# Optimization experiments

Hardware: AMD Instinct MI355X
Metric: run time of the kernel (lower is better)

Reference implementation:

```python
import jax, jax.numpy as jnp
import numpy as np

PI = float(np.pi)

def setup_inputs() -> dict:
    key = jax.random.key(0)
    k1, k2 = jax.random.split(key)
    inp = jax.random.normal(k1, (16, 4096, 512), dtype=jnp.float32)
    lengths = jax.random.randint(k2, (16,), 0, 4096, dtype=jnp.int32)
    return {"inp": inp, "lengths": lengths}

def reference(inp, lengths):
    B, S, D = inp.shape
    pos = jnp.arange(S, dtype=jnp.float32)                      # [S]
    lens = lengths.astype(jnp.float32)[:, None]                  # [B,1]
    safe_len = jnp.maximum(lens, 1.0)
    # cos(x / len * pi) for x < len, else 0 (matches torch.zeros init)
    pe = jnp.where(pos[None, :] < lens,
                   jnp.cos(pos[None, :] / safe_len * PI),
                   0.0)                                          # [B,S]
    pe = pe.astype(inp.dtype)
    # original intent: concatenate positional channel along feature dim
    return jnp.concatenate([inp, pe[:, :, None]], axis=2)        # [B,S,D+1]
```

## Files before the change

### kernel.cpp

```cpp
#include <hip/hip_runtime.h>
#include <hip/hip_bf16.h>
#include <math.h>


#define PB 16
#define PS 4096
#define PD 512
#define PI_F 3.14159265358979323846f

__global__ __launch_bounds__(256) void sinpe_kernel(
    const float* __restrict__ inp,
    const int* __restrict__ lengths,
    float* __restrict__ out)
{
    const int row = blockIdx.x;
    const int s   = row & (PS - 1);
    const int b   = row >> 12;

    const float* __restrict__ in_row  = inp + (size_t)row * PD;
    float* __restrict__       out_row = out + (size_t)row * (PD + 1);

    const int t = threadIdx.x;

    out_row[t]       = in_row[t];
    out_row[t + 256] = in_row[t + 256];

    if (t == 0) {
        const int len = lengths[b];
        float pe = 0.0f;
        if (s < len) {
            const float fl = fmaxf((float)len, 1.0f);
            pe = cosf(((float)s / fl) * PI_F);
        }
        out_row[PD] = pe;
    }
}

extern "C" void kernel_launch(void* const* d_in, const int* in_sizes, int n_in,
                              void* d_out, int out_size, void* d_ws, size_t ws_size,
                              hipStream_t stream)
{
    const float* inp     = (const float*)d_in[0];
    const int*   lengths = (const int*)d_in[1];
    float*       out     = (float*)d_out;

    const int n_rows = PB * PS;
    sinpe_kernel<<<n_rows, 256, 0, stream>>>(inp, lengths, out);
}
```

Measured before the change: 222.4 us.

## Process four rows per block with aligned float4 output stores

Each block now handles four rows, whose 2052 output floats form a 16-byte-aligned span. That span is written as 513 float4 stores, and each store gathers its four input values with scalar loads, handling row boundaries and the positional channel in a slow path. The aim is to replace unaligned scalar stores with wide aligned writes and to cut the block count by four. In exchange, input loads stay scalar and misaligned relative to the output, and one thread does a tail iteration on its own.

Result: slower. 233.7 us (+5.0%).

```diff
diff --git a/kernel.cpp b/kernel.cpp
--- a/kernel.cpp
+++ b/kernel.cpp
@@ -1,11 +1,11 @@
 #include <hip/hip_runtime.h>
-#include <hip/hip_bf16.h>
 #include <math.h>
 
 
 #define PB 16
 #define PS 4096
 #define PD 512
+#define PDO 513
 #define PI_F 3.14159265358979323846f
 
 __global__ __launch_bounds__(256) void sinpe_kernel(
@@ -13,27 +13,52 @@
     const int* __restrict__ lengths,
     float* __restrict__ out)
 {
-    const int row = blockIdx.x;
-    const int s   = row & (PS - 1);
-    const int b   = row >> 12;
-
-    const float* __restrict__ in_row  = inp + (size_t)row * PD;
-    float* __restrict__       out_row = out + (size_t)row * (PD + 1);
+    const int blk  = blockIdx.x;
+    const int row0 = blk << 2;
+    const float* __restrict__ in_base = inp + (size_t)row0 * PD;
+    float4* __restrict__ out_base = (float4*)(out + (size_t)row0 * PDO);
 
     const int t = threadIdx.x;
 
-    out_row[t]       = in_row[t];
-    out_row[t + 256] = in_row[t + 256];
+    auto process = [&](int q) {
+        const int l0 = q << 2;
+        const int r  = (l0 >= 3 * PDO) ? 3 : (l0 >= 2 * PDO) ? 2 : (l0 >= PDO) ? 1 : 0;
+        const int c0 = l0 - r * PDO;
 
-    if (t == 0) {
-        const int len = lengths[b];
-        float pe = 0.0f;
-        if (s < len) {
-            const float fl = fmaxf((float)len, 1.0f);
-            pe = cosf(((float)s / fl) * PI_F);
+        float4 v;
+        if (c0 <= PD - 4) {
+            const float* __restrict__ p = in_base + r * PD + c0;
+            v.x = p[0]; v.y = p[1]; v.z = p[2]; v.w = p[3];
+        } else {
+            float tmp[4];
+#pragma unroll
+            for (int j = 0; j < 4; ++j) {
+                int c  = c0 + j;
+                int rr = r;
+                if (c >= PDO) { c -= PDO; ++rr; }
+                if (c < PD) {
+                    tmp[j] = in_base[rr * PD + c];
+                } else {
+                    const int grow = row0 + rr;
+                    const int s    = grow & (PS - 1);
+                    const int b    = grow >> 12;
+                    const int len  = lengths[b];
+                    float pe = 0.0f;
+                    if (s < len) {
+                        const float fl = fmaxf((float)len, 1.0f);
+                        pe = cosf(((float)s / fl) * PI_F);
+                    }
+                    tmp[j] = pe;
+                }
+            }
+            v.x = tmp[0]; v.y = tmp[1]; v.z = tmp[2]; v.w = tmp[3];
         }
-        out_row[PD] = pe;
-    }
+        out_base[q] = v;
+    };
+
+    process(t);
+    process(t + 256);
+    if (t == 0) process(512);
 }
 
 extern "C" void kernel_launch(void* const* d_in, const int* in_sizes, int n_in,
@@ -44,6 +69,6 @@
     const int*   lengths = (const int*)d_in[1];
     float*       out     = (float*)d_out;
 
-    const int n_rows = PB * PS;
-    sinpe_kernel<<<n_rows, 256, 0, stream>>>(inp, lengths, out);
+    const int n_blocks = (PB * PS) / 4;
+    sinpe_kernel<<<n_blocks, 256, 0, stream>>>(inp, lengths, out);
 }
```

## Stage 16 rows in swizzled LDS to emit fully vectorized float4 output

Applied to the files above, without the earlier changes.

Each block now handles 16 rows. It loads the input with float4 reads into registers, writes them into shared memory with an XOR swizzle that avoids bank conflicts, and appends the cosine positional values. It then reassembles the 513-wide output rows so every store is an aligned float4. This removes the misaligned scalar stores that the odd row stride forced and cuts the number of blocks by 16x. The cost is 33KB of LDS per block, a block barrier, and index arithmetic with a magic-number division in the emit loop.

Result: slower. 232.8 us (+4.7%).

```diff
diff --git a/kernel.cpp b/kernel.cpp
--- a/kernel.cpp
+++ b/kernel.cpp
@@ -1,39 +1,96 @@
 #include <hip/hip_runtime.h>
-#include <hip/hip_bf16.h>
 #include <math.h>
 
 
-#define PB 16
-#define PS 4096
-#define PD 512
+#define PB   16
+#define PS   4096
+#define PD   512
+#define PDO  513
+#define ROWS 16
+#define TPB  256
+#define IN_DW  (ROWS * PD)
+#define IMG_DW (IN_DW + ROWS)
+#define OUT_V4 ((ROWS * PDO) / 4)
 #define PI_F 3.14159265358979323846f
 
-__global__ __launch_bounds__(256) void sinpe_kernel(
+__device__ __forceinline__ int phi(int idx) {
+    return idx ^ ((idx >> 5) & 3);
+}
+
+__global__ __launch_bounds__(TPB) void sinpe_kernel(
     const float* __restrict__ inp,
     const int* __restrict__ lengths,
     float* __restrict__ out)
 {
-    const int row = blockIdx.x;
-    const int s   = row & (PS - 1);
-    const int b   = row >> 12;
+    __shared__ float lds[IMG_DW];
 
-    const float* __restrict__ in_row  = inp + (size_t)row * PD;
-    float* __restrict__       out_row = out + (size_t)row * (PD + 1);
+    const int blk  = blockIdx.x;
+    const int row0 = blk * ROWS;
+    const int t    = threadIdx.x;
 
-    const int t = threadIdx.x;
+    const float4* __restrict__ in4  = (const float4*)(inp + (size_t)row0 * PD);
+    float4* __restrict__       out4 = (float4*)(out + (size_t)row0 * PDO);
 
-    out_row[t]       = in_row[t];
-    out_row[t + 256] = in_row[t + 256];
+    float4 v[8];
+#pragma unroll
+    for (int i = 0; i < 8; ++i)
+        v[i] = in4[t + i * TPB];
 
-    if (t == 0) {
-        const int len = lengths[b];
+    if (t < ROWS) {
+        const int grow = row0 + t;
+        const int s    = grow & (PS - 1);
+        const int b    = grow >> 12;
+        const int len  = lengths[b];
         float pe = 0.0f;
         if (s < len) {
             const float fl = fmaxf((float)len, 1.0f);
             pe = cosf(((float)s / fl) * PI_F);
         }
-        out_row[PD] = pe;
+        const int idx = IN_DW + t;
+        lds[phi(idx)] = pe;
     }
+
+    const int x  = (t >> 3) & 3;
+    const bool b0 = (x & 1) != 0;
+    const bool b1 = (x & 2) != 0;
+#pragma unroll
+    for (int i = 0; i < 8; ++i) {
+        const int k = t + i * TPB;
+        float a0 = v[i].x, a1 = v[i].y, a2 = v[i].z, a3 = v[i].w;
+        float s0 = b0 ? a1 : a0;
+        float s1 = b0 ? a0 : a1;
+        float s2 = b0 ? a3 : a2;
+        float s3 = b0 ? a2 : a3;
+        float4 w;
+        w.x = b1 ? s2 : s0;
+        w.y = b1 ? s3 : s1;
+        w.z = b1 ? s0 : s2;
+        w.w = b1 ? s1 : s3;
+        *(float4*)&lds[4 * k] = w;
+    }
+
+    __syncthreads();
+
+    auto emit = [&](int q) {
+        float tmp[4];
+#pragma unroll
+        for (int j = 0; j < 4; ++j) {
+            const int l = 4 * q + j;
+            const int r = (int)(((unsigned)l * 8177u) >> 22);
+            const int c = l - PDO * r;
+            const int idx = (c < PD) ? (l - r) : (IN_DW + r);
+            tmp[j] = lds[phi(idx)];
+        }
+        float4 o;
+        o.x = tmp[0]; o.y = tmp[1]; o.z = tmp[2]; o.w = tmp[3];
+        out4[q] = o;
+    };
+
+#pragma unroll
+    for (int i = 0; i < 8; ++i)
+        emit(t + i * TPB);
+    if (t < OUT_V4 - 8 * TPB)
+        emit(t + 8 * TPB);
 }
 
 extern "C" void kernel_launch(void* const* d_in, const int* in_sizes, int n_in,
@@ -44,6 +101,6 @@
     const int*   lengths = (const int*)d_in[1];
     float*       out     = (float*)d_out;
 
-    const int n_rows = PB * PS;
-    sinpe_kernel<<<n_rows, 256, 0, stream>>>(inp, lengths, out);
+    const int n_blocks = (PB * PS) / ROWS;
+    sinpe_kernel<<<n_blocks, TPB, 0, stream>>>(inp, lengths, out);
 }
```

## Write output as aligned float4 stream with shifted-window input reconstruction

Applied to the files above, without the earlier changes.

Replaces the one-block-per-row scalar copy with a flat grid in which each thread produces aligned float4 chunks of the 513-wide output. Each chunk is rebuilt from two neighbouring float4 input loads, selected by the row-dependent misalignment, and the positional cosine is inserted when the chunk covers a row end. This is meant to turn scalar, misaligned stores into full-width vector stores and to cut the number of blocks. In exchange every chunk issues a redundant second load, and the index math depends on a magic-number division that must be exact.

New measurement: 232.0 us. +4.3%, slower.

```diff
diff --git a/kernel.cpp b/kernel.cpp
--- a/kernel.cpp
+++ b/kernel.cpp
@@ -1,38 +1,83 @@
 #include <hip/hip_runtime.h>
-#include <hip/hip_bf16.h>
 #include <math.h>
 
 
-#define PB 16
-#define PS 4096
-#define PD 512
+#define PS   4096
+#define PD   512
+#define PDO  513
 #define PI_F 3.14159265358979323846f
+#define OUT_V4 8404992
+#define IN_V4  8388608
+#define TPB  256
+#define CPT  4
 
-__global__ __launch_bounds__(256) void sinpe_kernel(
+__global__ __launch_bounds__(TPB) void sinpe_kernel(
     const float* __restrict__ inp,
     const int* __restrict__ lengths,
     float* __restrict__ out)
 {
-    const int row = blockIdx.x;
-    const int s   = row & (PS - 1);
-    const int b   = row >> 12;
+    const float4* __restrict__ in4  = (const float4*)inp;
+    float4* __restrict__       out4 = (float4*)out;
 
-    const float* __restrict__ in_row  = inp + (size_t)row * PD;
-    float* __restrict__       out_row = out + (size_t)row * (PD + 1);
+    const int q0 = blockIdx.x * (TPB * CPT) + threadIdx.x;
 
-    const int t = threadIdx.x;
+    float4 cur[CPT], prv[CPT];
+    int r_[CPT], c0_[CPT];
 
-    out_row[t]       = in_row[t];
-    out_row[t + 256] = in_row[t + 256];
+#pragma unroll
+    for (int k = 0; k < CPT; ++k) {
+        const int q  = q0 + k * TPB;
+        const int l0 = q << 2;
+        const int r  = (int)__umulhi((unsigned)l0, 8372256u);
+        const int c0 = l0 - r * PDO;
+        const int sh = r >> 2;
+        const int si = q - sh;
+        int ci = si;     if (ci > IN_V4 - 1) ci = IN_V4 - 1;
+        int pi = si - 1; if (pi < 0)         pi = 0;
+        cur[k] = in4[ci];
+        prv[k] = in4[pi];
+        r_[k] = r; c0_[k] = c0;
+    }
 
-    if (t == 0) {
-        const int len = lengths[b];
-        float pe = 0.0f;
-        if (s < len) {
-            const float fl = fmaxf((float)len, 1.0f);
-            pe = cosf(((float)s / fl) * PI_F);
+#pragma unroll
+    for (int k = 0; k < CPT; ++k) {
+        const int q   = q0 + k * TPB;
+        const int r   = r_[k];
+        const int c0  = c0_[k];
+        const int dlt = r & 3;
+
+        const float px = prv[k].x, py = prv[k].y, pz = prv[k].z, pw = prv[k].w;
+        const float cx = cur[k].x, cy = cur[k].y, cz = cur[k].z, cw = cur[k].w;
+        const bool d2 = (dlt & 2) != 0;
+        const bool d1 = (dlt & 1) != 0;
+        const float Am1 = d2 ? py : pw;
+        const float A0  = d2 ? pz : cx;
+        const float A1  = d2 ? pw : cy;
+        const float A2  = d2 ? cx : cz;
+        const float A3  = d2 ? cy : cw;
+        float w0 = d1 ? Am1 : A0;
+        float w1 = d1 ? A0  : A1;
+        float w2 = d1 ? A1  : A2;
+        float w3 = d1 ? A2  : A3;
+
+        if (c0 >= 509) {
+            const int mpe = 512 - c0;
+            const int b   = r >> 12;
+            const int s   = r & (PS - 1);
+            const int len = lengths[b];
+            float pe = 0.0f;
+            if (s < len)
+                pe = cosf(((float)s / fmaxf((float)len, 1.0f)) * PI_F);
+            const float n0 = (mpe == 0) ? pe : w0;
+            const float n1 = (mpe == 1) ? pe : ((mpe < 1) ? w0 : w1);
+            const float n2 = (mpe == 2) ? pe : ((mpe < 2) ? w1 : w2);
+            const float n3 = (mpe == 3) ? pe : w2;
+            w0 = n0; w1 = n1; w2 = n2; w3 = n3;
         }
-        out_row[PD] = pe;
+
+        float4 o;
+        o.x = w0; o.y = w1; o.z = w2; o.w = w3;
+        out4[q] = o;
     }
 }
 
@@ -44,6 +89,6 @@
     const int*   lengths = (const int*)d_in[1];
     float*       out     = (float*)d_out;
 
-    const int n_rows = PB * PS;
-    sinpe_kernel<<<n_rows, 256, 0, stream>>>(inp, lengths, out);
+    const int n_blocks = OUT_V4 / (TPB * CPT);
+    sinpe_kernel<<<n_blocks, TPB, 0, stream>>>(inp, lengths, out);
 }
```
